# Kernel optimization log

Hardware: AMD Instinct MI355X
Metric: run time of the kernel (lower is better)

Reference implementation:

```python
import jax, jax.numpy as jnp
import numpy as np

LAM = 0.1


def distance_corr(var_1, var_2, normedweight, power=1):
    # pairwise absolute-difference matrices [N, N]
    amat = jnp.abs(var_1[:, None] - var_1[None, :])
    bmat = jnp.abs(var_2[:, None] - var_2[None, :])
    # weighted row means (weight per column, as in torch broadcast)
    amatavg = jnp.mean(amat * normedweight, axis=1)
    Amat = amat - amatavg[None, :] - amatavg[:, None] + jnp.mean(amatavg * normedweight)
    bmatavg = jnp.mean(bmat * normedweight, axis=1)
    Bmat = bmat - bmatavg[None, :] - bmatavg[:, None] + jnp.mean(bmatavg * normedweight)
    ABavg = jnp.mean(Amat * Bmat * normedweight, axis=1)
    AAavg = jnp.mean(Amat * Amat * normedweight, axis=1)
    BBavg = jnp.mean(Bmat * Bmat * normedweight, axis=1)
    num = jnp.mean(ABavg * normedweight)
    den = jnp.mean(AAavg * normedweight) * jnp.mean(BBavg * normedweight)
    if power == 1:
        return num / jnp.sqrt(den)
    elif power == 2:
        return num ** 2 / den
    else:
        return (num / jnp.sqrt(den)) ** power


def reference(outputs, labels, event, weights):
    n = outputs.shape[0]
    # BCEWithLogits (reduction='none'): softplus(x) - x*y, numerically stable
    bce = (jnp.logaddexp(0.0, outputs) - outputs * labels) * weights
    bce_mean = jnp.mean(bce)
    normedweight = weights * n / jnp.sum(weights)
    disco = distance_corr(outputs, event, normedweight)
    tot = bce_mean + LAM * disco
    return (bce_mean, disco, tot)


def setup_inputs() -> dict:
    key = jax.random.key(0)
    k1, k2, k3, k4 = jax.random.split(key, 4)
    N = 8192
    return {
        "outputs": jax.random.normal(k1, (N,), dtype=jnp.float32),
        "labels": jax.random.uniform(k2, (N,), dtype=jnp.float32),
        "event": jax.random.normal(k3, (N,), dtype=jnp.float32),
        "weights": jax.random.uniform(k4, (N,), dtype=jnp.float32),
    }
```

## Files before the change

### kernel.cpp

```cpp
#include <hip/hip_runtime.h>
#include <math.h>


#define BLK  256
#define RPT  4
#define JLEN 128

__device__ inline double waveReduceD(double v) {
    for (int off = 32; off > 0; off >>= 1) v += __shfl_down(v, off, 64);
    return v;
}

__device__ inline double blockReduceD(double v, double* lds) {
    int lane = threadIdx.x & 63, wid = threadIdx.x >> 6;
    v = waveReduceD(v);
    if (lane == 0) lds[wid] = v;
    __syncthreads();
    double r = 0.0;
    if (wid == 0) {
        int nw = blockDim.x >> 6;
        r = (lane < nw) ? lds[lane] : 0.0;
        r = waveReduceD(r);
    }
    __syncthreads();
    return r;
}

__global__ __launch_bounds__(BLK) void kf(
        const float* __restrict__ x, const float* __restrict__ e,
        const float* __restrict__ w, int n, double* __restrict__ wsd,
        float* __restrict__ RA, float* __restrict__ RB) {
    __shared__ float xs[JLEN], es[JLEN], wsh[JLEN];
    __shared__ double lds[BLK / 64];
    int t = threadIdx.x;
    int j0 = blockIdx.y * JLEN;
    if (t < JLEN) {
        int j = j0 + t;
        xs[t] = x[j]; es[t] = e[j]; wsh[t] = w[j];
    }
    __syncthreads();

    int i0 = blockIdx.x * (BLK * RPT) + t;
    float xi[RPT], ei[RPT], ra[RPT], rb[RPT], ab[RPT], aa[RPT], bb[RPT];
#pragma unroll
    for (int r = 0; r < RPT; ++r) {
        int i = i0 + r * BLK;
        xi[r] = x[i]; ei[r] = e[i];
        ra[r] = 0.f; rb[r] = 0.f;
        ab[r] = 0.f; aa[r] = 0.f; bb[r] = 0.f;
    }

#pragma unroll 4
    for (int k = 0; k < JLEN; ++k) {
        float xj = xs[k], ej = es[k], wj = wsh[k];
#pragma unroll
        for (int r = 0; r < RPT; ++r) {
            float a  = fabsf(xi[r] - xj);
            float b  = fabsf(ei[r] - ej);
            float wa = wj * a;
            float wb = wj * b;
            ra[r] += wa;
            rb[r] += wb;
            ab[r] = fmaf(wa, b, ab[r]);
            aa[r] = fmaf(wa, a, aa[r]);
            bb[r] = fmaf(wb, b, bb[r]);
        }
    }

    double tab = 0.0, taa = 0.0, tbb = 0.0;
#pragma unroll
    for (int r = 0; r < RPT; ++r) {
        float wi = w[i0 + r * BLK];
        tab += (double)(wi * ab[r]);
        taa += (double)(wi * aa[r]);
        tbb += (double)(wi * bb[r]);
    }
    tab = blockReduceD(tab, lds);
    taa = blockReduceD(taa, lds);
    tbb = blockReduceD(tbb, lds);
    if (t == 0) {
        atomicAdd(&wsd[0], tab);
        atomicAdd(&wsd[1], taa);
        atomicAdd(&wsd[2], tbb);
    }
#pragma unroll
    for (int r = 0; r < RPT; ++r) {
        atomicAdd(&RA[i0 + r * BLK], ra[r]);
        atomicAdd(&RB[i0 + r * BLK], rb[r]);
    }
}

__global__ __launch_bounds__(1024) void kg(
        const float* __restrict__ x, const float* __restrict__ lab,
        const float* __restrict__ w, const float* __restrict__ RA,
        const float* __restrict__ RB, int n, const double* __restrict__ wsd,
        float* __restrict__ out) {
    __shared__ double lds[16];
    double sW = 0, sBCE = 0, sAB = 0, sAA = 0, sBB = 0, sCA = 0, sCB = 0;
    for (int i = threadIdx.x; i < n; i += blockDim.x) {
        float wi = w[i];
        float xi = x[i], yi = lab[i];
        float sp = fmaxf(xi, 0.f) + log1pf(expf(-fabsf(xi)));
        float rai = RA[i], rbi = RB[i];
        sW   += (double)wi;
        sBCE += (double)((sp - xi * yi) * wi);
        double wra = (double)wi * rai;
        double wrb = (double)wi * rbi;
        sAB += wra * rbi;
        sAA += wra * rai;
        sBB += wrb * rbi;
        sCA += wra;
        sCB += wrb;
    }
    sW   = blockReduceD(sW, lds);
    sBCE = blockReduceD(sBCE, lds);
    sAB  = blockReduceD(sAB, lds);
    sAA  = blockReduceD(sAA, lds);
    sBB  = blockReduceD(sBB, lds);
    sCA  = blockReduceD(sCA, lds);
    sCB  = blockReduceD(sCB, lds);
    if (threadIdx.x == 0) {
        double N  = (double)n;
        double s  = N / sW;
        double s2 = s * s, s3 = s2 * s, s4 = s2 * s2;
        double Sab = s2 * wsd[0] - (2.0 * s3 / N) * sAB + (s4 / (N * N)) * sCA * sCB;
        double Saa = s2 * wsd[1] - (2.0 * s3 / N) * sAA + (s4 / (N * N)) * sCA * sCA;
        double Sbb = s2 * wsd[2] - (2.0 * s3 / N) * sBB + (s4 / (N * N)) * sCB * sCB;
        double disco = Sab / sqrt(Saa * Sbb);
        double bce   = sBCE / N;
        out[0] = (float)bce;
        out[1] = (float)disco;
        out[2] = (float)(bce + 0.1 * disco);
    }
}

extern "C" void kernel_launch(void* const* d_in, const int* in_sizes, int n_in,
                              void* d_out, int out_size, void* d_ws, size_t ws_size,
                              hipStream_t stream) {
    const float* outputs = (const float*)d_in[0];
    const float* labels  = (const float*)d_in[1];
    const float* event   = (const float*)d_in[2];
    const float* weights = (const float*)d_in[3];
    int n = in_sizes[0];

    double* wsd = (double*)d_ws;
    float* RA = (float*)((char*)d_ws + 64);
    float* RB = RA + n;
    float* out = (float*)d_out;

    hipMemsetAsync(d_ws, 0, 64 + (size_t)2 * n * sizeof(float), stream);

    dim3 gF(n / (BLK * RPT), n / JLEN);
    kf<<<gF, BLK, 0, stream>>>(outputs, event, weights, n, wsd, RA, RB);
    kg<<<1, 1024, 0, stream>>>(outputs, labels, weights, RA, RB, n, wsd, out);
}
```

Before: 107.3 us.

## Replace atomics with partial buffers, derive AA/BB closed-form, split final reduction

The pairwise kernel no longer accumulates the weighted |dx|^2 and |de|^2 sums. These are now computed in closed form from weighted moments of x and e (sum |xi-xj|^2 = 2(W*Sxx - Sx^2)). This drops two FMAs and two accumulators from the inner loop, and JLEN is halved to double the grid. Float atomics on the row sums are replaced by per-tile partial writes, and the single-block finisher becomes a multi-block reduction plus a small final kernel, removing the memset. In exchange it adds workspace traffic of njs*n partials and one extra kernel launch.

```diff
diff --git a/kernel.cpp b/kernel.cpp
--- a/kernel.cpp
+++ b/kernel.cpp
@@ -4,7 +4,8 @@
 
 #define BLK  256
 #define RPT  4
-#define JLEN 128
+#define JLEN 64
+#define NSC  12
 
 __device__ inline double waveReduceD(double v) {
     for (int off = 32; off > 0; off >>= 1) v += __shfl_down(v, off, 64);
@@ -28,26 +29,25 @@
 
 __global__ __launch_bounds__(BLK) void kf(
         const float* __restrict__ x, const float* __restrict__ e,
-        const float* __restrict__ w, int n, double* __restrict__ wsd,
-        float* __restrict__ RA, float* __restrict__ RB) {
+        const float* __restrict__ w, int n, double* __restrict__ tpart,
+        float* __restrict__ RAp, float* __restrict__ RBp) {
     __shared__ float xs[JLEN], es[JLEN], wsh[JLEN];
     __shared__ double lds[BLK / 64];
     int t = threadIdx.x;
-    int j0 = blockIdx.y * JLEN;
+    int tj = blockIdx.y;
+    int j0 = tj * JLEN;
     if (t < JLEN) {
-        int j = j0 + t;
-        xs[t] = x[j]; es[t] = e[j]; wsh[t] = w[j];
+        xs[t] = x[j0 + t]; es[t] = e[j0 + t]; wsh[t] = w[j0 + t];
     }
     __syncthreads();
 
     int i0 = blockIdx.x * (BLK * RPT) + t;
-    float xi[RPT], ei[RPT], ra[RPT], rb[RPT], ab[RPT], aa[RPT], bb[RPT];
+    float xi[RPT], ei[RPT], ra[RPT], rb[RPT], ab[RPT];
 #pragma unroll
     for (int r = 0; r < RPT; ++r) {
         int i = i0 + r * BLK;
         xi[r] = x[i]; ei[r] = e[i];
-        ra[r] = 0.f; rb[r] = 0.f;
-        ab[r] = 0.f; aa[r] = 0.f; bb[r] = 0.f;
+        ra[r] = 0.f; rb[r] = 0.f; ab[r] = 0.f;
     }
 
 #pragma unroll 4
@@ -55,79 +55,86 @@
         float xj = xs[k], ej = es[k], wj = wsh[k];
 #pragma unroll
         for (int r = 0; r < RPT; ++r) {
-            float a  = fabsf(xi[r] - xj);
-            float b  = fabsf(ei[r] - ej);
-            float wa = wj * a;
-            float wb = wj * b;
-            ra[r] += wa;
-            rb[r] += wb;
-            ab[r] = fmaf(wa, b, ab[r]);
-            aa[r] = fmaf(wa, a, aa[r]);
-            bb[r] = fmaf(wb, b, bb[r]);
+            float a = fabsf(xi[r] - xj);
+            float b = fabsf(ei[r] - ej);
+            ra[r] = fmaf(wj, a, ra[r]);
+            rb[r] = fmaf(wj, b, rb[r]);
+            ab[r] = fmaf(wj, a * b, ab[r]);
         }
     }
 
-    double tab = 0.0, taa = 0.0, tbb = 0.0;
+    double tab = 0.0;
 #pragma unroll
     for (int r = 0; r < RPT; ++r) {
-        float wi = w[i0 + r * BLK];
-        tab += (double)(wi * ab[r]);
-        taa += (double)(wi * aa[r]);
-        tbb += (double)(wi * bb[r]);
+        int i = i0 + r * BLK;
+        tab += (double)(w[i] * ab[r]);
+        RAp[(size_t)tj * n + i] = ra[r];
+        RBp[(size_t)tj * n + i] = rb[r];
     }
     tab = blockReduceD(tab, lds);
-    taa = blockReduceD(taa, lds);
-    tbb = blockReduceD(tbb, lds);
-    if (t == 0) {
-        atomicAdd(&wsd[0], tab);
-        atomicAdd(&wsd[1], taa);
-        atomicAdd(&wsd[2], tbb);
+    if (t == 0) tpart[blockIdx.y * gridDim.x + blockIdx.x] = tab;
+}
+
+__global__ __launch_bounds__(256) void kg1(
+        const float* __restrict__ x, const float* __restrict__ lab,
+        const float* __restrict__ e, const float* __restrict__ w,
+        const float* __restrict__ RAp, const float* __restrict__ RBp,
+        int n, int njs, const double* __restrict__ tpart, int ntp,
+        double* __restrict__ spart) {
+    __shared__ double lds[4];
+    int t = threadIdx.x;
+    int i = blockIdx.x * 256 + t;
+    double rai = 0.0, rbi = 0.0;
+    for (int p = 0; p < njs; ++p) {
+        rai += (double)RAp[(size_t)p * n + i];
+        rbi += (double)RBp[(size_t)p * n + i];
     }
+    double wi = (double)w[i];
+    double xi = (double)x[i], ei = (double)e[i], yi = (double)lab[i];
+    float xf = x[i];
+    float sp = fmaxf(xf, 0.f) + log1pf(expf(-fabsf(xf)));
+    double acc[NSC];
+    acc[0]  = wi;
+    acc[1]  = ((double)sp - xi * yi) * wi;
+    acc[2]  = wi * rai * rbi;
+    acc[3]  = wi * rai * rai;
+    acc[4]  = wi * rbi * rbi;
+    acc[5]  = wi * rai;
+    acc[6]  = wi * rbi;
+    acc[7]  = wi * xi;
+    acc[8]  = wi * xi * xi;
+    acc[9]  = wi * ei;
+    acc[10] = wi * ei * ei;
+    acc[11] = (i < ntp) ? tpart[i] : 0.0;
 #pragma unroll
-    for (int r = 0; r < RPT; ++r) {
-        atomicAdd(&RA[i0 + r * BLK], ra[r]);
-        atomicAdd(&RB[i0 + r * BLK], rb[r]);
+    for (int k = 0; k < NSC; ++k) {
+        double r = blockReduceD(acc[k], lds);
+        if (t == 0) spart[blockIdx.x * NSC + k] = r;
     }
 }
 
-__global__ __launch_bounds__(1024) void kg(
-        const float* __restrict__ x, const float* __restrict__ lab,
-        const float* __restrict__ w, const float* __restrict__ RA,
-        const float* __restrict__ RB, int n, const double* __restrict__ wsd,
-        float* __restrict__ out) {
-    __shared__ double lds[16];
-    double sW = 0, sBCE = 0, sAB = 0, sAA = 0, sBB = 0, sCA = 0, sCB = 0;
-    for (int i = threadIdx.x; i < n; i += blockDim.x) {
-        float wi = w[i];
-        float xi = x[i], yi = lab[i];
-        float sp = fmaxf(xi, 0.f) + log1pf(expf(-fabsf(xi)));
-        float rai = RA[i], rbi = RB[i];
-        sW   += (double)wi;
-        sBCE += (double)((sp - xi * yi) * wi);
-        double wra = (double)wi * rai;
-        double wrb = (double)wi * rbi;
-        sAB += wra * rbi;
-        sAA += wra * rai;
-        sBB += wrb * rbi;
-        sCA += wra;
-        sCB += wrb;
-    }
-    sW   = blockReduceD(sW, lds);
-    sBCE = blockReduceD(sBCE, lds);
-    sAB  = blockReduceD(sAB, lds);
-    sAA  = blockReduceD(sAA, lds);
-    sBB  = blockReduceD(sBB, lds);
-    sCA  = blockReduceD(sCA, lds);
-    sCB  = blockReduceD(sCB, lds);
-    if (threadIdx.x == 0) {
-        double N  = (double)n;
-        double s  = N / sW;
-        double s2 = s * s, s3 = s2 * s, s4 = s2 * s2;
-        double Sab = s2 * wsd[0] - (2.0 * s3 / N) * sAB + (s4 / (N * N)) * sCA * sCB;
-        double Saa = s2 * wsd[1] - (2.0 * s3 / N) * sAA + (s4 / (N * N)) * sCA * sCA;
-        double Sbb = s2 * wsd[2] - (2.0 * s3 / N) * sBB + (s4 / (N * N)) * sCB * sCB;
+__global__ __launch_bounds__(NSC * 32) void kg2(
+        const double* __restrict__ spart, int nblk, int n, float* __restrict__ out) {
+    __shared__ double sk[NSC];
+    int t = threadIdx.x;
+    int k = t >> 5, p = t & 31;
+    double v = (k < NSC && p < nblk) ? spart[p * NSC + k] : 0.0;
+    for (int off = 16; off > 0; off >>= 1) v += __shfl_down(v, off, 32);
+    if (p == 0 && k < NSC) sk[k] = v;
+    __syncthreads();
+    if (t == 0) {
+        double W = sk[0], BCE = sk[1], AB = sk[2], AA = sk[3], BB = sk[4];
+        double CA = sk[5], CB = sk[6], Sx = sk[7], Sxx = sk[8];
+        double Se = sk[9], See = sk[10], T1ab = sk[11];
+        double N = (double)n;
+        double T1aa = 2.0 * (W * Sxx - Sx * Sx);
+        double T1bb = 2.0 * (W * See - Se * Se);
+        double s = N / W, s2 = s * s, s3 = s2 * s, s4 = s2 * s2;
+        double Sab = s2 * T1ab - (2.0 * s3 / N) * AB + (s4 / (N * N)) * CA * CB;
+        double Saa = s2 * T1aa - (2.0 * s3 / N) * AA + (s4 / (N * N)) * CA * CA;
+        double Sbb = s2 * T1bb - (2.0 * s3 / N) * BB + (s4 / (N * N)) * CB * CB;
         double disco = Sab / sqrt(Saa * Sbb);
-        double bce   = sBCE / N;
+        double bce = BCE / N;
         out[0] = (float)bce;
         out[1] = (float)disco;
         out[2] = (float)(bce + 0.1 * disco);
@@ -143,14 +150,20 @@
     const float* weights = (const float*)d_in[3];
     int n = in_sizes[0];
 
-    double* wsd = (double*)d_ws;
-    float* RA = (float*)((char*)d_ws + 64);
-    float* RB = RA + n;
+    int njs = n / JLEN;
+    int nit = n / (BLK * RPT);
+    int ntp = njs * nit;
+    int nblk1 = n / 256;
+
+    double* tpart = (double*)d_ws;
+    float* RAp = (float*)((char*)d_ws + 16384);
+    float* RBp = RAp + (size_t)njs * n;
+    double* spart = (double*)((char*)d_ws + 16384 + (size_t)2 * njs * n * sizeof(float));
     float* out = (float*)d_out;
 
-    hipMemsetAsync(d_ws, 0, 64 + (size_t)2 * n * sizeof(float), stream);
-
-    dim3 gF(n / (BLK * RPT), n / JLEN);
-    kf<<<gF, BLK, 0, stream>>>(outputs, event, weights, n, wsd, RA, RB);
-    kg<<<1, 1024, 0, stream>>>(outputs, labels, weights, RA, RB, n, wsd, out);
+    dim3 gF(nit, njs);
+    kf<<<gF, BLK, 0, stream>>>(outputs, event, weights, n, tpart, RAp, RBp);
+    kg1<<<nblk1, 256, 0, stream>>>(outputs, labels, event, weights, RAp, RBp,
+                                   n, njs, tpart, ntp, spart);
+    kg2<<<1, NSC * 32, 0, stream>>>(spart, nblk1, n, out);
 }
```

New measurement: 117.0 us. +9.0%, slower.
